# Optimization experiments

Hardware: AMD Instinct MI355X
Metric: run time of the kernel (lower is better)

Reference implementation:

```python
import jax, jax.numpy as jnp
import numpy as np
import math

EPS_NORM = 1e-12
BN_EPS = 1e-5


def _l2norm(x):
    n = jnp.sqrt(jnp.sum(x * x, axis=-1, keepdims=True))
    return x / jnp.maximum(n, EPS_NORM)


def setup_inputs() -> dict:
    key = jax.random.key(0)
    ks = jax.random.split(key, 16)
    b, c, t, l = 16, 32, 16, 256
    s = 0.05
    return {
        "x": jax.random.normal(ks[0], (b, c, t, l), jnp.float32),
        "q_w": jax.random.normal(ks[1], (c, c), jnp.float32) * s,
        "q_b": jax.random.normal(ks[2], (c,), jnp.float32) * s,
        "k_w": jax.random.normal(ks[3], (c, c), jnp.float32) * s,
        "k_b": jax.random.normal(ks[4], (c,), jnp.float32) * s,
        "v_w": jax.random.normal(ks[5], (c, c), jnp.float32) * s,
        "v_b": jax.random.normal(ks[6], (c,), jnp.float32) * s,
        "m_w": jax.random.normal(ks[7], (c, c), jnp.float32) * s,
        "m_b": jax.random.normal(ks[8], (c,), jnp.float32) * s,
        "pre_prompt": jax.random.normal(ks[9], (1, c, 1, l), jnp.float32) * s,
        "conv_w": jax.random.normal(ks[10], (c, c, 9, 1), jnp.float32) * s,
        "conv_b": jax.random.normal(ks[11], (c,), jnp.float32) * s,
        "bn_gamma": jnp.ones((c,), jnp.float32),
        "bn_beta": jnp.zeros((c,), jnp.float32),
        "lin_w": jax.random.normal(ks[12], (l, l), jnp.float32) * s,
        "lin_b": jax.random.normal(ks[13], (l,), jnp.float32) * s,
        "atten_flag": 1,
    }


def reference(x, q_w, q_b, k_w, k_b, v_w, v_b, m_w, m_b, pre_prompt,
              conv_w, conv_b, bn_gamma, bn_beta, lin_w, lin_b, atten_flag):
    b, c, t, l = x.shape
    nh = 8
    hd = c // nh

    xp = jnp.transpose(x, (0, 2, 3, 1))  # (b,t,l,c)

    def heads(w, bias):
        h = xp @ w.T + bias
        h = h.reshape(b, t, l, nh, hd).transpose(0, 1, 3, 2, 4)  # (b,t,nh,l,hd)
        return _l2norm(h)

    q = heads(q_w, q_b)
    k = heads(k_w, k_b)
    v = heads(v_w, v_b)

    atten = jnp.einsum('bthld,bthmd->bthlm', q, k) / math.sqrt(hd)
    atten = jax.nn.softmax(atten, axis=-1)
    o = jnp.einsum('bthlm,bthmd->bthld', atten, v)  # (b,t,nh,l,hd)
    o = o.transpose(0, 1, 3, 2, 4).reshape(b, t, l, c)
    o = o @ m_w.T + m_b
    xo = jnp.transpose(o, (0, 3, 1, 2))  # (b,c,t,l)

    pre = jnp.broadcast_to(pre_prompt, (b, c, 1, l))
    con = jnp.concatenate([xo[:, :, :8], pre], axis=2)  # (b,c,9,l)

    # ConvNormAct: Conv2d (VALID, kernel (9,1)) + BatchNorm2d (batch stats) + ReLU
    h = jax.lax.conv_general_dilated(
        con, conv_w, window_strides=(1, 1), padding='VALID',
        dimension_numbers=('NCHW', 'OIHW', 'NCHW'))  # (b,c,1,l)
    h = h + conv_b[None, :, None, None]
    mean = jnp.mean(h, axis=(0, 2, 3), keepdims=True)
    var = jnp.var(h, axis=(0, 2, 3), keepdims=True)
    h = (h - mean) * jax.lax.rsqrt(var + BN_EPS)
    h = h * bn_gamma[None, :, None, None] + bn_beta[None, :, None, None]
    h = jax.nn.relu(h)

    p = h @ lin_w.T + lin_b  # Linear over token_len axis
    p = xo[:, :, 2:3] - p
    return jnp.concatenate([xo[:, :, :8], p], axis=2)  # (b,c,9,l)
```

## Files before the change

kernel.cpp:

```cpp
#include <hip/hip_runtime.h>
#include <hip/hip_bf16.h>


#define XF_OFF 0u
#define WF_OFF 8388608u
#define O_OFF  8738688u
#define H_OFF  10835840u
#define S_OFF  11360128u

#define QW   0
#define QB   1024
#define KW   1056
#define KB   2080
#define VW   2112
#define VB   3136
#define MW   3168
#define MB   4192
#define PREo 4224
#define CWo  12416
#define CBo  21632
#define GAMo 21664
#define BETo 21696
#define LWo  21728
#define LBo  87264
#define WF_N 87520

__device__ __forceinline__ int probe_f32(const unsigned short* graw) {
    return graw[0] == 0;
}
__device__ __forceinline__ float ld_any(const void* p, long i, int f32) {
    if (f32) return ((const float*)p)[i];
    union { unsigned int u; float f; } c;
    c.u = ((unsigned int)((const unsigned short*)p)[i]) << 16;
    return c.f;
}
__device__ __forceinline__ void st_out(void* out, size_t i, float v, int f32) {
    if (f32) ((float*)out)[i] = v;
    else ((__hip_bfloat16*)out)[i] = __float2bfloat16(v);
}
__device__ __forceinline__ float ld_out(const void* out, size_t i, int f32) {
    return ld_any(out, (long)i, f32);
}
__device__ __forceinline__ float bflo(unsigned int u) {
    union { unsigned int i; float f; } c; c.i = u << 16; return c.f;
}
__device__ __forceinline__ float bfhi(unsigned int u) {
    union { unsigned int i; float f; } c; c.i = u & 0xffff0000u; return c.f;
}
__device__ __forceinline__ unsigned short f2bs(float f) {
    union { __hip_bfloat16 b; unsigned short s; } c; c.b = __float2bfloat16(f); return c.s;
}

__global__ __launch_bounds__(256) void k_ingest_x(
    const void* __restrict__ x, float* __restrict__ xf,
    const unsigned short* __restrict__ graw)
{
    const int f32 = probe_f32(graw);
    const int n = 16 * 32 * 16 * 256;
    for (int i = blockIdx.x * 256 + threadIdx.x; i < n; i += gridDim.x * 256)
        xf[i] = ld_any(x, i, f32);
}

__global__ __launch_bounds__(256) void k_ingest_p(
    const void* qw, const void* qb, const void* kw, const void* kb,
    const void* vw, const void* vb, const void* mw, const void* mb,
    const void* pre, const void* cw, const void* cb,
    const void* gam, const void* bet, const void* lw, const void* lb,
    float* __restrict__ wf, float* __restrict__ s,
    const unsigned short* __restrict__ graw)
{
    const int f32 = probe_f32(graw);
    const int tid = threadIdx.x;
    if (blockIdx.x == 0 && tid < 64) s[tid] = 0.0f;

    const void* srcs[15] = {qw,qb,kw,kb,vw,vb,mw,mb,pre,cw,cb,gam,bet,lw,lb};
    const int starts[16] = {QW,QB,KW,KB,VW,VB,MW,MB,PREo,CWo,CBo,GAMo,BETo,LWo,LBo,WF_N};

    int idx = blockIdx.x * 256 + tid;
    if (idx >= WF_N) return;
    int seg = 0;
    #pragma unroll
    for (int j = 1; j < 15; j++) if (idx >= starts[j]) seg = j;
    wf[idx] = ld_any(srcs[seg], idx - starts[seg], f32);
}

__global__ __launch_bounds__(256) void k_attn_fused(
    const float* __restrict__ xf, const float* __restrict__ wf,
    unsigned short* __restrict__ O)
{
    __shared__ float4 kk[256];
    __shared__ float4 vv[256];
    __shared__ float  wgt[3][4][32];
    __shared__ float  bia[3][4];

    const int tid = threadIdx.x;
    const int blk = blockIdx.x;
    const int h  = blk & 7;
    const int bt = blk >> 3;
    const int b  = bt >> 3, t = bt & 7;

    for (int e = tid; e < 384; e += 256) {
        int p = e >> 7, r = e & 127;
        int base = (p == 0) ? QW : ((p == 1) ? KW : VW);
        wgt[p][r >> 5][r & 31] = wf[base + (h * 4 + (r >> 5)) * 32 + (r & 31)];
    }
    if (tid < 12) {
        int p = tid >> 2, r = tid & 3;
        int base = (p == 0) ? QB : ((p == 1) ? KB : VB);
        bia[p][r] = wf[base + h * 4 + r];
    }

    float xv[32];
    #pragma unroll
    for (int c = 0; c < 32; c++)
        xv[c] = xf[(((long)b * 32 + c) * 16 + t) * 256 + tid];

    __syncthreads();

    float4 pr[3];
    #pragma unroll
    for (int p = 0; p < 3; p++) {
        float r0 = bia[p][0], r1 = bia[p][1], r2 = bia[p][2], r3 = bia[p][3];
        #pragma unroll
        for (int c = 0; c < 32; c++) {
            float xc = xv[c];
            r0 = fmaf(xc, wgt[p][0][c], r0);
            r1 = fmaf(xc, wgt[p][1][c], r1);
            r2 = fmaf(xc, wgt[p][2][c], r2);
            r3 = fmaf(xc, wgt[p][3][c], r3);
        }
        float s2 = r0*r0 + r1*r1 + r2*r2 + r3*r3;
        float inv = 1.0f / fmaxf(sqrtf(s2), 1e-12f);
        if (p == 0) inv *= 0.7213475204444817f;
        pr[p] = make_float4(r0*inv, r1*inv, r2*inv, r3*inv);
    }
    kk[tid] = pr[1];
    vv[tid] = pr[2];
    float4 q = pr[0];
    __syncthreads();

    float ox = 0.f, oy = 0.f, oz = 0.f, ow = 0.f, den = 0.f;
    #pragma unroll 8
    for (int m = 0; m < 256; m++) {
        float4 k4 = kk[m];
        float s = q.x * k4.x + q.y * k4.y;
        s = fmaf(q.z, k4.z, s);
        s = fmaf(q.w, k4.w, s);
        float e = exp2f(s);
        float4 v4 = vv[m];
        den += e;
        ox = fmaf(e, v4.x, ox);
        oy = fmaf(e, v4.y, oy);
        oz = fmaf(e, v4.z, oz);
        ow = fmaf(e, v4.w, ow);
    }
    float inv = 1.0f / den;

    unsigned short us[4] = { f2bs(ox*inv), f2bs(oy*inv), f2bs(oz*inv), f2bs(ow*inv) };
    uint2 pk;
    pk.x = (unsigned int)us[0] | ((unsigned int)us[1] << 16);
    pk.y = (unsigned int)us[2] | ((unsigned int)us[3] << 16);
    *(uint2*)(O + ((size_t)bt * 256u + tid) * 32u + h * 4u) = pk;
}

__global__ __launch_bounds__(256) void k_mproj(
    const unsigned short* __restrict__ O, const float* __restrict__ wf,
    void* __restrict__ out, const unsigned short* __restrict__ graw)
{
    __shared__ float w[1024];
    __shared__ float bias[32];
    const int f32 = probe_f32(graw);
    const int tid = threadIdx.x;
    const int blk = blockIdx.x;
    const int b = blk >> 3, t = blk & 7;

    #pragma unroll
    for (int ii = 0; ii < 4; ii++) w[tid + 256*ii] = wf[MW + tid + 256*ii];
    if (tid < 32) bias[tid] = wf[MB + tid];
    __syncthreads();

    float ov[32];
    const unsigned short* src = O + ((size_t)blk * 256u + tid) * 32u;
    #pragma unroll
    for (int cc = 0; cc < 4; cc++) {
        uint4 u = *(const uint4*)(src + cc * 8);
        unsigned int uu[4] = {u.x, u.y, u.z, u.w};
        #pragma unroll
        for (int j = 0; j < 4; j++) {
            ov[cc*8 + 2*j]     = bflo(uu[j]);
            ov[cc*8 + 2*j + 1] = bfhi(uu[j]);
        }
    }

    for (int co = 0; co < 32; co++) {
        float s = bias[co];
        #pragma unroll
        for (int c = 0; c < 32; c++) s = fmaf(ov[c], w[co*32 + c], s);
        st_out(out, (((size_t)b * 32 + co) * 9 + t) * 256u + tid, s, f32);
    }
}

__global__ __launch_bounds__(256) void k_conv(
    const void* __restrict__ out, const float* __restrict__ wf,
    float* __restrict__ hout, float* __restrict__ s,
    const unsigned short* __restrict__ graw)
{
    __shared__ float w[4][32][9];
    const int f32 = probe_f32(graw);
    const int tid = threadIdx.x;
    const int blk = blockIdx.x;
    const int b = blk >> 3, co0 = (blk & 7) * 4;

    for (int e = tid; e < 1152; e += 256) {
        int g = e / 288, r = e % 288;
        w[g][r / 9][r % 9] = wf[CWo + (co0 + g) * 288 + r];
    }
    __syncthreads();

    const int l = tid;
    float a0 = 0.f, a1 = 0.f, a2 = 0.f, a3 = 0.f;
    for (int ci = 0; ci < 32; ci++) {
        size_t xob = (((size_t)b * 32 + ci) * 9) * 256u + l;
        float pv = wf[PREo + ci * 256 + l];
        #pragma unroll
        for (int kt = 0; kt < 9; kt++) {
            float v = (kt < 8) ? ld_out(out, xob + (size_t)kt * 256u, f32) : pv;
            a0 = fmaf(v, w[0][ci][kt], a0);
            a1 = fmaf(v, w[1][ci][kt], a1);
            a2 = fmaf(v, w[2][ci][kt], a2);
            a3 = fmaf(v, w[3][ci][kt], a3);
        }
    }
    a0 += wf[CBo + co0 + 0]; a1 += wf[CBo + co0 + 1];
    a2 += wf[CBo + co0 + 2]; a3 += wf[CBo + co0 + 3];

    hout[((size_t)b * 32 + co0 + 0) * 256u + l] = a0;
    hout[((size_t)b * 32 + co0 + 1) * 256u + l] = a1;
    hout[((size_t)b * 32 + co0 + 2) * 256u + l] = a2;
    hout[((size_t)b * 32 + co0 + 3) * 256u + l] = a3;

    float acc[4] = {a0, a1, a2, a3};
    #pragma unroll
    for (int g = 0; g < 4; g++) {
        float sg = acc[g], sq = acc[g] * acc[g];
        #pragma unroll
        for (int off = 32; off > 0; off >>= 1) {
            sg += __shfl_down(sg, off, 64);
            sq += __shfl_down(sq, off, 64);
        }
        if ((tid & 63) == 0) {
            atomicAdd(&s[co0 + g], sg);
            atomicAdd(&s[32 + co0 + g], sq);
        }
    }
}

__global__ __launch_bounds__(256) void k_lin(
    const float* __restrict__ hbuf, const float* __restrict__ s,
    const float* __restrict__ wf, void* __restrict__ out,
    const unsigned short* __restrict__ graw)
{
    __shared__ float hn[256];
    const int f32 = probe_f32(graw);
    const int tid = threadIdx.x;
    const int blk = blockIdx.x;
    const int b = blk >> 5, co = blk & 31;

    float mean = s[co] * (1.0f / 4096.0f);
    float var  = fmaxf(s[32 + co] * (1.0f / 4096.0f) - mean * mean, 0.0f);
    float sc = wf[GAMo + co] * __frsqrt_rn(var + 1e-5f);
    float sh = wf[BETo + co] - mean * sc;

    float hv = hbuf[(size_t)blk * 256u + tid];
    hn[tid] = fmaxf(fmaf(hv, sc, sh), 0.0f);
    __syncthreads();

    const float* rp = wf + LWo + (size_t)tid * 256u;
    float acc = 0.f;
    for (int i0 = 0; i0 < 256; i0 += 4) {
        float4 u = *(const float4*)(rp + i0);
        acc = fmaf(hn[i0+0], u.x, acc);
        acc = fmaf(hn[i0+1], u.y, acc);
        acc = fmaf(hn[i0+2], u.z, acc);
        acc = fmaf(hn[i0+3], u.w, acc);
    }
    acc += wf[LBo + tid];

    float xo2 = ld_out(out, (((size_t)b * 32 + co) * 9 + 2) * 256u + tid, f32);
    st_out(out, (((size_t)b * 32 + co) * 9 + 8) * 256u + tid, xo2 - acc, f32);
}

extern "C" void kernel_launch(void* const* d_in, const int* in_sizes, int n_in,
                              void* d_out, int out_size, void* d_ws, size_t ws_size,
                              hipStream_t stream) {
    const unsigned short* graw = (const unsigned short*)d_in[12];

    float* xf  = (float*)((char*)d_ws + XF_OFF);
    float* wfp = (float*)((char*)d_ws + WF_OFF);
    unsigned short* Obuf = (unsigned short*)((char*)d_ws + O_OFF);
    float* hbuf = (float*)((char*)d_ws + H_OFF);
    float* sbuf = (float*)((char*)d_ws + S_OFF);

    k_ingest_x  <<<2048, 256, 0, stream>>>(d_in[0], xf, graw);
    k_ingest_p  <<<342,  256, 0, stream>>>(d_in[1], d_in[2], d_in[3], d_in[4],
                                           d_in[5], d_in[6], d_in[7], d_in[8],
                                           d_in[9], d_in[10], d_in[11],
                                           d_in[12], d_in[13], d_in[14], d_in[15],
                                           wfp, sbuf, graw);
    k_attn_fused<<<1024, 256, 0, stream>>>(xf, wfp, Obuf);
    k_mproj     <<<128,  256, 0, stream>>>(Obuf, wfp, d_out, graw);
    k_conv      <<<128,  256, 0, stream>>>(d_out, wfp, hbuf, sbuf, graw);
    k_lin       <<<512,  256, 0, stream>>>(hbuf, sbuf, wfp, d_out, graw);
}
```

Baseline: 202.2 us.

## Read x directly in attention kernel, drop ingest pass, pack K/V as bf16

```diff
diff --git a/kernel.cpp b/kernel.cpp
--- a/kernel.cpp
+++ b/kernel.cpp
@@ -2,11 +2,10 @@
 #include <hip/hip_bf16.h>
 
 
-#define XF_OFF 0u
-#define WF_OFF 8388608u
-#define O_OFF  8738688u
-#define H_OFF  10835840u
-#define S_OFF  11360128u
+#define WF_OFF 0u
+#define O_OFF  350080u
+#define H_OFF  2447232u
+#define S_OFF  2971520u
 
 #define QW   0
 #define QB   1024
@@ -50,15 +49,8 @@
 __device__ __forceinline__ unsigned short f2bs(float f) {
     union { __hip_bfloat16 b; unsigned short s; } c; c.b = __float2bfloat16(f); return c.s;
 }
-
-__global__ __launch_bounds__(256) void k_ingest_x(
-    const void* __restrict__ x, float* __restrict__ xf,
-    const unsigned short* __restrict__ graw)
-{
-    const int f32 = probe_f32(graw);
-    const int n = 16 * 32 * 16 * 256;
-    for (int i = blockIdx.x * 256 + threadIdx.x; i < n; i += gridDim.x * 256)
-        xf[i] = ld_any(x, i, f32);
+__device__ __forceinline__ unsigned int pk2(float a, float b) {
+    return (unsigned int)f2bs(a) | ((unsigned int)f2bs(b) << 16);
 }
 
 __global__ __launch_bounds__(256) void k_ingest_p(
@@ -66,17 +58,13 @@
     const void* vw, const void* vb, const void* mw, const void* mb,
     const void* pre, const void* cw, const void* cb,
     const void* gam, const void* bet, const void* lw, const void* lb,
-    float* __restrict__ wf, float* __restrict__ s,
-    const unsigned short* __restrict__ graw)
-{
-    const int f32 = probe_f32(graw);
-    const int tid = threadIdx.x;
-    if (blockIdx.x == 0 && tid < 64) s[tid] = 0.0f;
-
+    float* __restrict__ wf, const unsigned short* __restrict__ graw)
+{
+    const int f32 = probe_f32(graw);
     const void* srcs[15] = {qw,qb,kw,kb,vw,vb,mw,mb,pre,cw,cb,gam,bet,lw,lb};
     const int starts[16] = {QW,QB,KW,KB,VW,VB,MW,MB,PREo,CWo,CBo,GAMo,BETo,LWo,LBo,WF_N};
 
-    int idx = blockIdx.x * 256 + tid;
+    int idx = blockIdx.x * 256 + threadIdx.x;
     if (idx >= WF_N) return;
     int seg = 0;
     #pragma unroll
@@ -85,19 +73,22 @@
 }
 
 __global__ __launch_bounds__(256) void k_attn_fused(
-    const float* __restrict__ xf, const float* __restrict__ wf,
-    unsigned short* __restrict__ O)
-{
-    __shared__ float4 kk[256];
-    __shared__ float4 vv[256];
-    __shared__ float  wgt[3][4][32];
-    __shared__ float  bia[3][4];
+    const void* __restrict__ x, const float* __restrict__ wf,
+    unsigned short* __restrict__ O, float* __restrict__ sbuf,
+    const unsigned short* __restrict__ graw)
+{
+    __shared__ uint4 kv[256];
+    __shared__ float wgt[3][4][32];
+    __shared__ float bia[3][4];
 
     const int tid = threadIdx.x;
     const int blk = blockIdx.x;
+    const int f32 = probe_f32(graw);
     const int h  = blk & 7;
     const int bt = blk >> 3;
     const int b  = bt >> 3, t = bt & 7;
+
+    if (blk == 0 && tid < 64) sbuf[tid] = 0.0f;
 
     for (int e = tid; e < 384; e += 256) {
         int p = e >> 7, r = e & 127;
@@ -111,9 +102,20 @@
     }
 
     float xv[32];
-    #pragma unroll
-    for (int c = 0; c < 32; c++)
-        xv[c] = xf[(((long)b * 32 + c) * 16 + t) * 256 + tid];
+    const long xbase = ((long)b * 32 * 16 + t) * 256 + tid;
+    if (f32) {
+        const float* xp = (const float*)x;
+        #pragma unroll
+        for (int c = 0; c < 32; c++) xv[c] = xp[xbase + (long)c * 4096];
+    } else {
+        const unsigned short* xp = (const unsigned short*)x;
+        #pragma unroll
+        for (int c = 0; c < 32; c++) {
+            union { unsigned int u; float f; } cc;
+            cc.u = ((unsigned int)xp[xbase + (long)c * 4096]) << 16;
+            xv[c] = cc.f;
+        }
+    }
 
     __syncthreads();
 
@@ -134,33 +136,33 @@
         if (p == 0) inv *= 0.7213475204444817f;
         pr[p] = make_float4(r0*inv, r1*inv, r2*inv, r3*inv);
     }
-    kk[tid] = pr[1];
-    vv[tid] = pr[2];
+    kv[tid] = make_uint4(pk2(pr[1].x, pr[1].y), pk2(pr[1].z, pr[1].w),
+                         pk2(pr[2].x, pr[2].y), pk2(pr[2].z, pr[2].w));
     float4 q = pr[0];
     __syncthreads();
 
     float ox = 0.f, oy = 0.f, oz = 0.f, ow = 0.f, den = 0.f;
     #pragma unroll 8
     for (int m = 0; m < 256; m++) {
-        float4 k4 = kk[m];
-        float s = q.x * k4.x + q.y * k4.y;
-        s = fmaf(q.z, k4.z, s);
-        s = fmaf(q.w, k4.w, s);
-        float e = exp2f(s);
-        float4 v4 = vv[m];
+        uint4 pk = kv[m];
+        float s = q.x * bflo(pk.x);
+        s = fmaf(q.y, bfhi(pk.x), s);
+        s = fmaf(q.z, bflo(pk.y), s);
+        s = fmaf(q.w, bfhi(pk.y), s);
+        float e = __builtin_amdgcn_exp2f(s);
         den += e;
-        ox = fmaf(e, v4.x, ox);
-        oy = fmaf(e, v4.y, oy);
-        oz = fmaf(e, v4.z, oz);
-        ow = fmaf(e, v4.w, ow);
+        ox = fmaf(e, bflo(pk.z), ox);
+        oy = fmaf(e, bfhi(pk.z), oy);
+        oz = fmaf(e, bflo(pk.w), oz);
+        ow = fmaf(e, bfhi(pk.w), ow);
     }
     float inv = 1.0f / den;
 
     unsigned short us[4] = { f2bs(ox*inv), f2bs(oy*inv), f2bs(oz*inv), f2bs(ow*inv) };
-    uint2 pk;
-    pk.x = (unsigned int)us[0] | ((unsigned int)us[1] << 16);
-    pk.y = (unsigned int)us[2] | ((unsigned int)us[3] << 16);
-    *(uint2*)(O + ((size_t)bt * 256u + tid) * 32u + h * 4u) = pk;
+    uint2 opk;
+    opk.x = (unsigned int)us[0] | ((unsigned int)us[1] << 16);
+    opk.y = (unsigned int)us[2] | ((unsigned int)us[3] << 16);
+    *(uint2*)(O + ((size_t)bt * 256u + tid) * 32u + h * 4u) = opk;
 }
 
 __global__ __launch_bounds__(256) void k_mproj(
@@ -295,19 +297,17 @@
                               hipStream_t stream) {
     const unsigned short* graw = (const unsigned short*)d_in[12];
 
-    float* xf  = (float*)((char*)d_ws + XF_OFF);
     float* wfp = (float*)((char*)d_ws + WF_OFF);
     unsigned short* Obuf = (unsigned short*)((char*)d_ws + O_OFF);
     float* hbuf = (float*)((char*)d_ws + H_OFF);
     float* sbuf = (float*)((char*)d_ws + S_OFF);
 
-    k_ingest_x  <<<2048, 256, 0, stream>>>(d_in[0], xf, graw);
     k_ingest_p  <<<342,  256, 0, stream>>>(d_in[1], d_in[2], d_in[3], d_in[4],
                                            d_in[5], d_in[6], d_in[7], d_in[8],
                                            d_in[9], d_in[10], d_in[11],
                                            d_in[12], d_in[13], d_in[14], d_in[15],
-                                           wfp, sbuf, graw);
-    k_attn_fused<<<1024, 256, 0, stream>>>(xf, wfp, Obuf);
+                                           wfp, graw);
+    k_attn_fused<<<1024, 256, 0, stream>>>(d_in[0], wfp, Obuf, sbuf, graw);
     k_mproj     <<<128,  256, 0, stream>>>(Obuf, wfp, d_out, graw);
     k_conv      <<<128,  256, 0, stream>>>(d_out, wfp, hbuf, sbuf, graw);
     k_lin       <<<512,  256, 0, stream>>>(hbuf, sbuf, wfp, d_out, graw);
```

Result: faster. 192.1 us (-5.0%).
